# Kernel tuning notes

Hardware: AMD Instinct MI355X
Metric: run time of the kernel (lower is better)

The kernel has to match this reference:

```python
import jax, jax.numpy as jnp
import numpy as np
import math

NHEAD = 8
OUT = 64
EF = 64
IN = 256
NTYPES = 5
NH = 50000
NT = 100000
E = 800000
NEG_SLOPE = 0.2

def _uniform(key, shape, fan):
    # matches reset(): uniform(-stdv, stdv), stdv = sqrt(6/(fan_in+fan_out)) over last two dims
    stdv = math.sqrt(6.0 / (shape[-2] + shape[-1]))
    return jax.random.uniform(key, shape, jnp.float32, -stdv, stdv)

def setup_inputs() -> dict:
    key = jax.random.key(0)
    ks = jax.random.split(key, 12)
    head_feature = jax.random.normal(ks[0], (NH, IN), jnp.float32)
    tail_feature = jax.random.normal(ks[1], (NT, IN), jnp.float32)
    head_ind = jax.random.randint(ks[2], (E,), 0, NH)
    tail_ind = jax.random.randint(ks[3], (E,), 0, NT)
    tmp_edge = jax.random.randint(ks[4], (E,), 0, NTYPES)
    edge_emb = _uniform(ks[5], (NTYPES, EF), None)
    W = _uniform(ks[6], (IN, OUT * NHEAD), None)
    W_e = _uniform(ks[7], (EF, EF * NHEAD), None)
    a_l = _uniform(ks[8], (1, NHEAD, OUT), None)
    a_r = _uniform(ks[9], (1, NHEAD, OUT), None)
    a_e = _uniform(ks[10], (1, NHEAD, EF), None)
    return {"head_feature": head_feature, "tail_feature": tail_feature,
            "head_ind": head_ind, "tail_ind": tail_ind, "tmp_edge": tmp_edge,
            "edge_emb": edge_emb, "W": W, "W_e": W_e,
            "a_l": a_l, "a_r": a_r, "a_e": a_e}

def reference(head_feature, tail_feature, head_ind, tail_ind, tmp_edge,
              edge_emb, W, W_e, a_l, a_r, a_e):
    n_head_nodes = head_feature.shape[0]
    # projections (dropout is identity in eval)
    h_head = (head_feature @ W).reshape(-1, NHEAD, OUT)   # [NH, H, D]
    h_tail = (tail_feature @ W).reshape(-1, NHEAD, OUT)   # [NT, H, D]
    e = (edge_emb @ W_e).reshape(-1, NHEAD, EF)           # [T, H, EF]
    # per-edge attention logits, all heads at once: [E, H]
    h_l = jnp.sum(a_l * h_head, axis=-1)[head_ind]
    h_r = jnp.sum(a_r * h_tail, axis=-1)[tail_ind]
    h_e = jnp.sum(a_e * e, axis=-1)[tmp_edge]
    att = jax.nn.leaky_relu(h_l + h_r + h_e, NEG_SLOPE)
    # sparse (per-destination-row) softmax, vectorized over heads
    seg_max = jax.ops.segment_max(att, head_ind, num_segments=n_head_nodes)
    att = jnp.exp(att - seg_max[head_ind])
    denom = jax.ops.segment_sum(att, head_ind, num_segments=n_head_nodes)
    att = att / denom[head_ind]                           # [E, H]
    # weighted aggregation per head (small fixed loop over heads)
    outs = [jax.ops.segment_sum(att[:, n:n + 1] * h_tail[tail_ind, n, :],
                                head_ind, num_segments=n_head_nodes)
            for n in range(NHEAD)]
    out = jnp.stack(outs, axis=1).reshape(n_head_nodes, -1)  # [NH, H*D]
    return out, att
```

## Files before the change

kernel.cpp:

```cpp
#include <hip/hip_runtime.h>

#define NH 50000
#define NT 100000
#define NE 800000
#define MPAD 100096

typedef __attribute__((ext_vector_type(8))) short bf16x8;
typedef __attribute__((ext_vector_type(4))) float f32x4;
typedef __attribute__((ext_vector_type(8))) unsigned short u16x8;

__device__ __forceinline__ unsigned short f2bf(float f){
  unsigned int u = __float_as_uint(f);
  u += 0x7FFFu + ((u >> 16) & 1u);
  return (unsigned short)(u >> 16);
}

__device__ __forceinline__ void fma8(float* acc, float w, uint4 pk){
  acc[0] += w*__uint_as_float(pk.x<<16); acc[1] += w*__uint_as_float(pk.x&0xFFFF0000u);
  acc[2] += w*__uint_as_float(pk.y<<16); acc[3] += w*__uint_as_float(pk.y&0xFFFF0000u);
  acc[4] += w*__uint_as_float(pk.z<<16); acc[5] += w*__uint_as_float(pk.z&0xFFFF0000u);
  acc[6] += w*__uint_as_float(pk.w<<16); acc[7] += w*__uint_as_float(pk.w&0xFFFF0000u);
}

__device__ __forceinline__ void gl2lds16(const unsigned short* g, unsigned short* l){
  __builtin_amdgcn_global_load_lds(
      (const __attribute__((address_space(1))) void*)g,
      (__attribute__((address_space(3))) void*)l, 16, 0, 0);
}

__global__ void k_prep(const float* __restrict__ W, const float* __restrict__ W_e,
                       const float* __restrict__ edge_emb,
                       const float* __restrict__ a_l, const float* __restrict__ a_r,
                       const float* __restrict__ a_e,
                       unsigned short* __restrict__ wlr_t,
                       float* __restrict__ h_e){
  __shared__ float s_al[512], s_ar[512], s_ae[512], s_wef[512];
  int t = threadIdx.x;
  for (int i=t;i<512;i+=256){ s_al[i]=a_l[i]; s_ar[i]=a_r[i]; s_ae[i]=a_e[i]; }
  __syncthreads();
  { int k = t;
    for (int h=0;h<8;h++){
      float accl=0.f, accr=0.f;
      for (int d=0; d<64; d++){
        float w = W[k*512 + h*64 + d];
        accl += w*s_al[h*64+d];
        accr += w*s_ar[h*64+d];
      }
      wlr_t[h*256 + k]     = f2bf(accl);
      wlr_t[(8+h)*256 + k] = f2bf(accr);
    }
  }
  if (t<64){
    for (int h=0;h<8;h++){
      float acc=0.f;
      for (int f=0; f<64; f++) acc += W_e[t*512 + h*64 + f]*s_ae[h*64+f];
      s_wef[t*8+h]=acc;
    }
  }
  __syncthreads();
  if (t<40){
    int ty=t>>3, h=t&7;
    float acc=0.f;
    for (int k2=0;k2<64;k2++) acc += edge_emb[ty*64+k2]*s_wef[k2*8+h];
    h_e[t]=acc;
  }
}

__global__ void k_wt(const float* __restrict__ W, unsigned short* __restrict__ Wt){
  int n = blockIdx.x, k = threadIdx.x;
  Wt[n*256+k] = f2bf(W[k*512+n]);
}

__global__ __launch_bounds__(256) void k_cvt(const float* __restrict__ A,
                                             unsigned short* __restrict__ Ab){
  size_t g = (size_t)blockIdx.x*256 + threadIdx.x;
  const float* src = A + g*8;
  float4 v0 = *(const float4*)(src);
  float4 v1 = *(const float4*)(src + 4);
  u16x8 s;
  s[0]=f2bf(v0.x); s[1]=f2bf(v0.y); s[2]=f2bf(v0.z); s[3]=f2bf(v0.w);
  s[4]=f2bf(v1.x); s[5]=f2bf(v1.y); s[6]=f2bf(v1.z); s[7]=f2bf(v1.w);
  *(u16x8*)(Ab + g*8) = s;
}

__global__ __launch_bounds__(256) void k_hl(const float* __restrict__ head_f,
      const unsigned short* __restrict__ wlr_t, float* __restrict__ h_l){
  __shared__ unsigned short As[256*64];
  __shared__ unsigned short Bs[16*256];
  int t = threadIdx.x;
  int wave = t>>6, lane = t&63;
  int lr = lane&15, lq = lane>>4;
  long r0 = (long)blockIdx.x*256;

#pragma unroll
  for (int i=0;i<2;i++){
    int q = i*256 + t;
    int c = q>>5, un = q&31;
    float4 v = *(const float4*)(wlr_t + c*256 + un*8);
    int u = un ^ (c&7);
    *(float4*)((char*)Bs + c*512 + u*16) = v;
  }

  f32x4 acc[4];
#pragma unroll
  for (int mf=0;mf<4;mf++) acc[mf]=(f32x4){0.f,0.f,0.f,0.f};

  for (int kt=0; kt<4; kt++){
    __syncthreads();
#pragma unroll
    for (int i=0;i<16;i++){
      int q = i*256+t;
      int row = q>>4, cg = q&15;
      long gr = r0 + row;
      float4 v = make_float4(0.f,0.f,0.f,0.f);
      if (gr < NH) v = *(const float4*)(head_f + gr*256 + kt*64 + cg*4);
      int u = (cg>>1) ^ (row&7);
      ushort4 sv;
      sv.x=f2bf(v.x); sv.y=f2bf(v.y); sv.z=f2bf(v.z); sv.w=f2bf(v.w);
      *(ushort4*)((char*)As + row*128 + u*16 + (cg&1)*8) = sv;
    }
    __syncthreads();
#pragma unroll
    for (int ks=0;ks<2;ks++){
      int un = kt*8 + ks*4 + lq;
      int cu = un ^ (lr&7);
      bf16x8 bfr = *(const bf16x8*)((const char*)Bs + lr*512 + cu*16);
#pragma unroll
      for (int mf=0;mf<4;mf++){
        int r = wave*64 + mf*16 + lr;
        int u = (ks*4+lq) ^ (r&7);
        bf16x8 afr = *(const bf16x8*)((const char*)As + r*128 + u*16);
        acc[mf] = __builtin_amdgcn_mfma_f32_16x16x32_bf16(afr, bfr, acc[mf], 0,0,0);
      }
    }
  }
#pragma unroll
  for (int mf=0;mf<4;mf++)
#pragma unroll
    for (int j=0;j<4;j++){
      long grow = r0 + wave*64 + mf*16 + lq*4 + j;
      if (grow < NH && lr < 8) h_l[grow*8+lr] = acc[mf][j];
    }
}

__global__ __launch_bounds__(256) void k_gemm2(const unsigned short* __restrict__ A_bf,
      const unsigned short* __restrict__ Wt, const float* __restrict__ a_r_g,
      unsigned short* __restrict__ Cout, float* __restrict__ h_r){
  __shared__ unsigned short As[2][128*64];
  __shared__ unsigned short Bs[2][128*64];
  int t = threadIdx.x;
  int wave = t>>6, lane = t&63;
  int lr = lane & 15, lq = lane >> 4;

  int bid = blockIdx.x;
  int wg  = (bid & 7)*391 + (bid >> 3);
  int m0 = (wg >> 2)*128;
  int n0 = (wg & 3)*128;

  auto STAGE = [&](int buf, int kt){
#pragma unroll
    for (int i=0;i<4;i++){
      int v = wave*256 + i*64 + lane;
      int row = v>>3, un = (v&7) ^ (row&7);
      gl2lds16(A_bf + (size_t)(m0+row)*256 + kt*64 + un*8,
               &As[buf][(wave*256 + i*64)*8]);
    }
#pragma unroll
    for (int i=0;i<4;i++){
      int v = wave*256 + i*64 + lane;
      int n = v>>3, un = (v&7) ^ (n&7);
      gl2lds16(Wt + (size_t)(n0+n)*256 + kt*64 + un*8,
               &Bs[buf][(wave*256 + i*64)*8]);
    }
  };

  int wm = (wave>>1)*64, wn = (wave&1)*64;

  f32x4 acc[4][4];
#pragma unroll
  for (int mf=0;mf<4;mf++)
#pragma unroll
    for (int nf=0;nf<4;nf++) acc[mf][nf] = (f32x4){0.f,0.f,0.f,0.f};

  STAGE(0, 0);
  __syncthreads();
  int cur = 0;
  for (int kt=0; kt<4; kt++){
    if (kt < 3) STAGE(cur^1, kt+1);

    bf16x8 af[2][4], bfr[2][4];
#pragma unroll
    for (int ks=0;ks<2;ks++)
#pragma unroll
      for (int mf=0;mf<4;mf++){
        int r = wm + mf*16 + lr;
        int u = (ks*4 + lq) ^ (r&7);
        af[ks][mf] = *(const bf16x8*)((const char*)As[cur] + r*128 + u*16);
      }
#pragma unroll
    for (int ks=0;ks<2;ks++)
#pragma unroll
      for (int nf=0;nf<4;nf++){
        int c = wn + nf*16 + lr;
        int u = (ks*4 + lq) ^ (c&7);
        bfr[ks][nf] = *(const bf16x8*)((const char*)Bs[cur] + c*128 + u*16);
      }
#pragma unroll
    for (int ks=0;ks<2;ks++)
#pragma unroll
      for (int mf=0;mf<4;mf++)
#pragma unroll
        for (int nf=0;nf<4;nf++)
          acc[mf][nf] = __builtin_amdgcn_mfma_f32_16x16x32_bf16(af[ks][mf], bfr[ks][nf], acc[mf][nf], 0,0,0);
    __syncthreads();
    cur ^= 1;
  }
#pragma unroll
  for (int mf=0;mf<4;mf++)
#pragma unroll
    for (int nf=0;nf<4;nf++){
      int gr = m0 + wm + mf*16 + lq*4;
      int gc = n0 + wn + nf*16 + lr;
#pragma unroll
      for (int j=0;j<4;j++)
        Cout[(size_t)(gr+j)*512 + gc] = f2bf(acc[mf][nf][j]);
    }
  {
    int h = (n0 + wn) >> 6;
    float w[4];
#pragma unroll
    for (int nf=0;nf<4;nf++) w[nf] = a_r_g[h*64 + nf*16 + lr];
#pragma unroll
    for (int mf=0;mf<4;mf++)
#pragma unroll
      for (int j=0;j<4;j++){
        float s = acc[mf][0][j]*w[0] + acc[mf][1][j]*w[1]
                + acc[mf][2][j]*w[2] + acc[mf][3][j]*w[3];
        s += __shfl_xor(s, 1); s += __shfl_xor(s, 2);
        s += __shfl_xor(s, 4); s += __shfl_xor(s, 8);
        int gr = m0 + wm + mf*16 + lq*4 + j;
        if (lr == 0 && gr < NT) h_r[(size_t)gr*8 + h] = s;
      }
  }
}

__global__ void k_hist(const int* __restrict__ head_ind, int* __restrict__ cnt){
  int e = blockIdx.x*256 + threadIdx.x;
  atomicAdd(&cnt[head_ind[e]], 1);
}

__global__ void k_scan1(const int* __restrict__ cnt, int* __restrict__ bsum){
  __shared__ int s[256];
  int b=blockIdx.x, t=threadIdx.x, g=b*256+t;
  s[t] = (g<NH)? cnt[g] : 0;
  __syncthreads();
  for (int off=128; off>0; off>>=1){ if (t<off) s[t]+=s[t+off]; __syncthreads(); }
  if (t==0) bsum[b]=s[0];
}
__global__ void k_scan2(int* __restrict__ bsum, int nb){
  __shared__ int s[256];
  int t=threadIdx.x;
  int v = (t<nb)? bsum[t] : 0;
  s[t]=v; __syncthreads();
  for (int off=1; off<256; off<<=1){
    int u = (t>=off)? s[t-off] : 0; __syncthreads();
    s[t]+=u; __syncthreads();
  }
  if (t<nb) bsum[t] = s[t]-v;
}
__global__ void k_scan3(const int* __restrict__ cnt, const int* __restrict__ bsum,
                        int* __restrict__ offs, int* __restrict__ cur){
  __shared__ int s[256];
  int b=blockIdx.x, t=threadIdx.x, g=b*256+t;
  int v=(g<NH)? cnt[g] : 0;
  s[t]=v; __syncthreads();
  for (int off=1; off<256; off<<=1){
    int u=(t>=off)? s[t-off] : 0; __syncthreads();
    s[t]+=u; __syncthreads();
  }
  int excl = s[t]-v + bsum[b];
  if (g<NH){
    offs[g]=excl; cur[g]=excl;
    if (g==NH-1) offs[NH]=excl+v;
  }
}

__global__ void k_logit2(const int* __restrict__ head_ind, const int* __restrict__ tail_ind,
                         const int* __restrict__ tmp_edge,
                         const float* __restrict__ h_l, const float* __restrict__ h_r,
                         const float* __restrict__ h_e,
                         int* __restrict__ cur,
                         float* __restrict__ att_csr,
                         int* __restrict__ edge_of, int* __restrict__ tail_s){
  int g = blockIdx.x*256 + threadIdx.x;
  int e = g>>3, h = g&7, l = threadIdx.x&63;
  int hd = head_ind[e], tl = tail_ind[e], ty = tmp_edge[e];
  float v = h_l[hd*8+h] + h_r[(size_t)tl*8+h] + h_e[ty*8+h];
  v = v > 0.f ? v : 0.2f*v;
  int p = 0;
  if (h==0) p = atomicAdd(&cur[hd], 1);
  p = __shfl(p, l & ~7);
  att_csr[p*8+h] = v;
  if (h==0){ edge_of[p]=e; tail_s[p]=tl; }
}

__global__ __launch_bounds__(256) void k_agg3(const int* __restrict__ offs,
      const int* __restrict__ edge_of, const int* __restrict__ tail_s,
      const float* __restrict__ att_csr,
      const unsigned short* __restrict__ h_tail,
      float* __restrict__ att, float* __restrict__ out){
  int t = threadIdx.x;
  int l = t & 63;
  int i = blockIdx.x*4 + (t>>6);
  int h = l & 7, hq = l >> 3;
  int s0 = offs[i];
  int deg = offs[i+1] - s0;

  float m = -1e30f;
  for (int q = hq; q < deg; q += 8) m = fmaxf(m, att_csr[(s0+q)*8 + h]);
  m = fmaxf(m, __shfl_xor(m, 8));
  m = fmaxf(m, __shfl_xor(m, 16));
  m = fmaxf(m, __shfl_xor(m, 32));
  float sum = 0.f;
  for (int q = hq; q < deg; q += 8) sum += __expf(att_csr[(s0+q)*8 + h] - m);
  sum += __shfl_xor(sum, 8); sum += __shfl_xor(sum, 16); sum += __shfl_xor(sum, 32);
  float r = (deg > 0) ? 1.f/sum : 0.f;

  float mh = __shfl(m, hq), rh = __shfl(r, hq);
  bool wlane = (l & 7) == 0;
  float acc[8];
#pragma unroll
  for (int c=0;c<8;c++) acc[c]=0.f;
  int j = 0;
  for (; j+4 <= deg; j += 4){
    int p0=s0+j, p1=p0+1, p2=p0+2, p3=p0+3;
    int t0=tail_s[p0], t1=tail_s[p1], t2=tail_s[p2], t3=tail_s[p3];
    float a0=att_csr[p0*8+hq], a1=att_csr[p1*8+hq];
    float a2=att_csr[p2*8+hq], a3=att_csr[p3*8+hq];
    uint4 r0 = *(const uint4*)(h_tail + (size_t)t0*512 + l*8);
    uint4 r1 = *(const uint4*)(h_tail + (size_t)t1*512 + l*8);
    uint4 r2 = *(const uint4*)(h_tail + (size_t)t2*512 + l*8);
    uint4 r3 = *(const uint4*)(h_tail + (size_t)t3*512 + l*8);
    float w0=__expf(a0-mh)*rh, w1=__expf(a1-mh)*rh;
    float w2=__expf(a2-mh)*rh, w3=__expf(a3-mh)*rh;
    if (wlane){
      __builtin_nontemporal_store(w0, &att[(size_t)edge_of[p0]*8 + hq]);
      __builtin_nontemporal_store(w1, &att[(size_t)edge_of[p1]*8 + hq]);
      __builtin_nontemporal_store(w2, &att[(size_t)edge_of[p2]*8 + hq]);
      __builtin_nontemporal_store(w3, &att[(size_t)edge_of[p3]*8 + hq]);
    }
    fma8(acc, w0, r0);
    fma8(acc, w1, r1);
    fma8(acc, w2, r2);
    fma8(acc, w3, r3);
  }
  for (; j < deg; j++){
    int p0 = s0+j;
    int t0 = tail_s[p0];
    float a0 = att_csr[p0*8 + hq];
    uint4 r0 = *(const uint4*)(h_tail + (size_t)t0*512 + l*8);
    float w0 = __expf(a0 - mh) * rh;
    if (wlane) __builtin_nontemporal_store(w0, &att[(size_t)edge_of[p0]*8 + hq]);
    fma8(acc, w0, r0);
  }
  float* o = out + (size_t)i*512 + l*8;
  f32x4 v0 = {acc[0],acc[1],acc[2],acc[3]};
  f32x4 v1 = {acc[4],acc[5],acc[6],acc[7]};
  __builtin_nontemporal_store(v0, (f32x4*)o);
  __builtin_nontemporal_store(v1, (f32x4*)(o+4));
}

extern "C" void kernel_launch(void* const* d_in, const int* in_sizes, int n_in,
                              void* d_out, int out_size, void* d_ws, size_t ws_size,
                              hipStream_t stream) {
  const float* head_f   = (const float*)d_in[0];
  const float* tail_f   = (const float*)d_in[1];
  const int*   head_ind = (const int*)d_in[2];
  const int*   tail_ind = (const int*)d_in[3];
  const int*   tmp_edge = (const int*)d_in[4];
  const float* edge_emb = (const float*)d_in[5];
  const float* W        = (const float*)d_in[6];
  const float* W_e      = (const float*)d_in[7];
  const float* a_l      = (const float*)d_in[8];
  const float* a_r      = (const float*)d_in[9];
  const float* a_e      = (const float*)d_in[10];

  float* out = (float*)d_out;
  float* att = out + (size_t)NH*512;
  unsigned short* A_bf = (unsigned short*)d_out;

  char* ws = (char*)d_ws;
  auto alloc = [&](size_t bytes)->char*{ char* p = ws; ws += (bytes+511)&~(size_t)511; return p; };
  unsigned short* Wt    = (unsigned short*)alloc((size_t)512*256*2);
  unsigned short* wlr_t = (unsigned short*)alloc((size_t)16*256*2);
  float* h_e            = (float*)alloc(512);
  float* h_l            = (float*)alloc((size_t)NH*8*4);
  float* h_r            = (float*)alloc((size_t)NT*8*4);
  unsigned short* h_tail= (unsigned short*)alloc((size_t)MPAD*512*2);
  int* cnt              = (int*)alloc((size_t)NH*4);
  int* offs             = (int*)alloc((size_t)(NH+1)*4);
  int* cur              = (int*)alloc((size_t)NH*4);
  int* bsum             = (int*)alloc(1024);
  int* edge_of          = (int*)alloc((size_t)NE*4);
  int* tail_s           = (int*)alloc((size_t)NE*4);
  float* att_csr        = (float*)alloc((size_t)NE*8*4);

  hipMemsetAsync(cnt, 0, (size_t)NH*4, stream);
  k_prep<<<1,256,0,stream>>>(W, W_e, edge_emb, a_l, a_r, a_e, wlr_t, h_e);
  k_wt<<<512,256,0,stream>>>(W, Wt);
  k_cvt<<<12500,256,0,stream>>>(tail_f, A_bf);
  k_hl<<<(NH+255)/256,256,0,stream>>>(head_f, wlr_t, h_l);
  k_gemm2<<<3128,256,0,stream>>>(A_bf, Wt, a_r, h_tail, h_r);
  k_hist<<<NE/256,256,0,stream>>>(head_ind, cnt);
  k_scan1<<<196,256,0,stream>>>(cnt, bsum);
  k_scan2<<<1,256,0,stream>>>(bsum, 196);
  k_scan3<<<196,256,0,stream>>>(cnt, bsum, offs, cur);
  k_logit2<<<NE*8/256,256,0,stream>>>(head_ind, tail_ind, tmp_edge, h_l, h_r, h_e,
                                      cur, att_csr, edge_of, tail_s);
  k_agg3<<<NH/4,256,0,stream>>>(offs, edge_of, tail_s, att_csr, h_tail, att, out);
}
```

Before: 436.8 us.

## Load GEMM B operand to registers, stage C via LDS, deepen gather unroll

The tail GEMM now reads the W operand straight from global memory into registers, prefetching the next k-tile, and no longer stages it through LDS. This halves shared memory use and drops the B-side LDS reads. The GEMM output is written through a swizzled LDS tile so it can be stored as coalesced 16-byte rows instead of scattered 2-byte stores. The aggregation loop is unrolled to 8 edges, with all gathers issued before any use, to raise memory-level parallelism. The cost is higher register pressure in both kernels, and B fragments are reloaded per wave from L2 rather than shared.

```diff
diff --git a/kernel.cpp b/kernel.cpp
--- a/kernel.cpp
+++ b/kernel.cpp
@@ -143,11 +143,10 @@
     }
 }
 
-__global__ __launch_bounds__(256) void k_gemm2(const unsigned short* __restrict__ A_bf,
+__global__ __launch_bounds__(256) void k_gemm3(const unsigned short* __restrict__ A_bf,
       const unsigned short* __restrict__ Wt, const float* __restrict__ a_r_g,
       unsigned short* __restrict__ Cout, float* __restrict__ h_r){
   __shared__ unsigned short As[2][128*64];
-  __shared__ unsigned short Bs[2][128*64];
   int t = threadIdx.x;
   int wave = t>>6, lane = t&63;
   int lr = lane & 15, lq = lane >> 4;
@@ -156,24 +155,6 @@
   int wg  = (bid & 7)*391 + (bid >> 3);
   int m0 = (wg >> 2)*128;
   int n0 = (wg & 3)*128;
-
-  auto STAGE = [&](int buf, int kt){
-#pragma unroll
-    for (int i=0;i<4;i++){
-      int v = wave*256 + i*64 + lane;
-      int row = v>>3, un = (v&7) ^ (row&7);
-      gl2lds16(A_bf + (size_t)(m0+row)*256 + kt*64 + un*8,
-               &As[buf][(wave*256 + i*64)*8]);
-    }
-#pragma unroll
-    for (int i=0;i<4;i++){
-      int v = wave*256 + i*64 + lane;
-      int n = v>>3, un = (v&7) ^ (n&7);
-      gl2lds16(Wt + (size_t)(n0+n)*256 + kt*64 + un*8,
-               &Bs[buf][(wave*256 + i*64)*8]);
-    }
-  };
-
   int wm = (wave>>1)*64, wn = (wave&1)*64;
 
   f32x4 acc[4][4];
@@ -182,49 +163,57 @@
 #pragma unroll
     for (int nf=0;nf<4;nf++) acc[mf][nf] = (f32x4){0.f,0.f,0.f,0.f};
 
-  STAGE(0, 0);
+  bf16x8 bcur[8], bnxt[8];
+
+#define STAGEA(buf, kt) do { \
+    _Pragma("unroll") \
+    for (int i=0;i<4;i++){ \
+      int v = wave*256 + i*64 + lane; \
+      int row = v>>3, un = (v&7) ^ (row&7); \
+      gl2lds16(A_bf + (size_t)(m0+row)*256 + (kt)*64 + un*8, \
+               &As[buf][(wave*256 + i*64)*8]); \
+    } } while(0)
+
+#define LOADB(kt, dst) do { \
+    _Pragma("unroll") \
+    for (int ks=0;ks<2;ks++) \
+      _Pragma("unroll") \
+      for (int nf=0;nf<4;nf++){ \
+        int c = wn + nf*16 + lr; \
+        (dst)[ks*4+nf] = *(const bf16x8*)(Wt + (size_t)(n0+c)*256 + ((kt)*8+ks*4+lq)*8); \
+      } } while(0)
+
+  STAGEA(0, 0);
+  LOADB(0, bcur);
   __syncthreads();
   int cur = 0;
   for (int kt=0; kt<4; kt++){
-    if (kt < 3) STAGE(cur^1, kt+1);
-
-    bf16x8 af[2][4], bfr[2][4];
-#pragma unroll
-    for (int ks=0;ks<2;ks++)
+    if (kt < 3){ STAGEA(cur^1, kt+1); LOADB(kt+1, bnxt); }
+#pragma unroll
+    for (int ks=0;ks<2;ks++){
+      bf16x8 af[4];
 #pragma unroll
       for (int mf=0;mf<4;mf++){
         int r = wm + mf*16 + lr;
         int u = (ks*4 + lq) ^ (r&7);
-        af[ks][mf] = *(const bf16x8*)((const char*)As[cur] + r*128 + u*16);
+        af[mf] = *(const bf16x8*)((const char*)As[cur] + r*128 + u*16);
       }
 #pragma unroll
-    for (int ks=0;ks<2;ks++)
-#pragma unroll
-      for (int nf=0;nf<4;nf++){
-        int c = wn + nf*16 + lr;
-        int u = (ks*4 + lq) ^ (c&7);
-        bfr[ks][nf] = *(const bf16x8*)((const char*)Bs[cur] + c*128 + u*16);
-      }
-#pragma unroll
-    for (int ks=0;ks<2;ks++)
-#pragma unroll
       for (int mf=0;mf<4;mf++)
 #pragma unroll
         for (int nf=0;nf<4;nf++)
-          acc[mf][nf] = __builtin_amdgcn_mfma_f32_16x16x32_bf16(af[ks][mf], bfr[ks][nf], acc[mf][nf], 0,0,0);
+          acc[mf][nf] = __builtin_amdgcn_mfma_f32_16x16x32_bf16(af[mf], bcur[ks*4+nf], acc[mf][nf], 0,0,0);
+    }
     __syncthreads();
-    cur ^= 1;
-  }
-#pragma unroll
-  for (int mf=0;mf<4;mf++)
-#pragma unroll
-    for (int nf=0;nf<4;nf++){
-      int gr = m0 + wm + mf*16 + lq*4;
-      int gc = n0 + wn + nf*16 + lr;
-#pragma unroll
-      for (int j=0;j<4;j++)
-        Cout[(size_t)(gr+j)*512 + gc] = f2bf(acc[mf][nf][j]);
-    }
+    if (kt < 3){
+      cur ^= 1;
+#pragma unroll
+      for (int i=0;i<8;i++) bcur[i] = bnxt[i];
+    }
+  }
+#undef STAGEA
+#undef LOADB
+
   {
     int h = (n0 + wn) >> 6;
     float w[4];
@@ -241,6 +230,26 @@
         int gr = m0 + wm + mf*16 + lq*4 + j;
         if (lr == 0 && gr < NT) h_r[(size_t)gr*8 + h] = s;
       }
+  }
+
+  unsigned short* Cs = &As[0][0];
+#pragma unroll
+  for (int mf=0;mf<4;mf++)
+#pragma unroll
+    for (int nf=0;nf<4;nf++)
+#pragma unroll
+      for (int j=0;j<4;j++){
+        int row = wm + mf*16 + lq*4 + j;
+        int cb  = (wn + nf*16 + lr)*2;
+        *(unsigned short*)((char*)Cs + row*256 + (cb ^ ((row&12)<<3))) = f2bf(acc[mf][nf][j]);
+      }
+  __syncthreads();
+#pragma unroll
+  for (int i=0;i<8;i++){
+    int v = i*256 + t;
+    int row = v>>4, u = v&15;
+    uint4 val = *(const uint4*)((const char*)Cs + row*256 + ((u*16) ^ ((row&12)<<3)));
+    *(uint4*)(Cout + (size_t)(m0+row)*512 + n0 + u*8) = val;
   }
 }
 
@@ -331,30 +340,36 @@
   float acc[8];
 #pragma unroll
   for (int c=0;c<8;c++) acc[c]=0.f;
+
   int j = 0;
-  for (; j+4 <= deg; j += 4){
-    int p0=s0+j, p1=p0+1, p2=p0+2, p3=p0+3;
-    int t0=tail_s[p0], t1=tail_s[p1], t2=tail_s[p2], t3=tail_s[p3];
+  for (; j+8 <= deg; j += 8){
+    int   tt[8]; float aa[8]; uint4 rr[8];
+#pragma unroll
+    for (int q2=0;q2<8;q2++){ int p=s0+j+q2; tt[q2]=tail_s[p]; aa[q2]=att_csr[p*8+hq]; }
+#pragma unroll
+    for (int q2=0;q2<8;q2++) rr[q2] = *(const uint4*)(h_tail + (size_t)tt[q2]*512 + l*8);
+#pragma unroll
+    for (int q2=0;q2<8;q2++){
+      float w = __expf(aa[q2]-mh)*rh;
+      if (wlane) __builtin_nontemporal_store(w, &att[(size_t)edge_of[s0+j+q2]*8 + hq]);
+      fma8(acc, w, rr[q2]);
+    }
+  }
+  for (; j+2 <= deg; j += 2){
+    int p0=s0+j, p1=p0+1;
+    int t0=tail_s[p0], t1=tail_s[p1];
     float a0=att_csr[p0*8+hq], a1=att_csr[p1*8+hq];
-    float a2=att_csr[p2*8+hq], a3=att_csr[p3*8+hq];
     uint4 r0 = *(const uint4*)(h_tail + (size_t)t0*512 + l*8);
     uint4 r1 = *(const uint4*)(h_tail + (size_t)t1*512 + l*8);
-    uint4 r2 = *(const uint4*)(h_tail + (size_t)t2*512 + l*8);
-    uint4 r3 = *(const uint4*)(h_tail + (size_t)t3*512 + l*8);
     float w0=__expf(a0-mh)*rh, w1=__expf(a1-mh)*rh;
-    float w2=__expf(a2-mh)*rh, w3=__expf(a3-mh)*rh;
     if (wlane){
       __builtin_nontemporal_store(w0, &att[(size_t)edge_of[p0]*8 + hq]);
       __builtin_nontemporal_store(w1, &att[(size_t)edge_of[p1]*8 + hq]);
-      __builtin_nontemporal_store(w2, &att[(size_t)edge_of[p2]*8 + hq]);
-      __builtin_nontemporal_store(w3, &att[(size_t)edge_of[p3]*8 + hq]);
     }
     fma8(acc, w0, r0);
     fma8(acc, w1, r1);
-    fma8(acc, w2, r2);
-    fma8(acc, w3, r3);
-  }
-  for (; j < deg; j++){
+  }
+  if (j < deg){
     int p0 = s0+j;
     int t0 = tail_s[p0];
     float a0 = att_csr[p0*8 + hq];
@@ -410,7 +425,7 @@
   k_wt<<<512,256,0,stream>>>(W, Wt);
   k_cvt<<<12500,256,0,stream>>>(tail_f, A_bf);
   k_hl<<<(NH+255)/256,256,0,stream>>>(head_f, wlr_t, h_l);
-  k_gemm2<<<3128,256,0,stream>>>(A_bf, Wt, a_r, h_tail, h_r);
+  k_gemm3<<<3128,256,0,stream>>>(A_bf, Wt, a_r, h_tail, h_r);
   k_hist<<<NE/256,256,0,stream>>>(head_ind, cnt);
   k_scan1<<<196,256,0,stream>>>(cnt, bsum);
   k_scan2<<<1,256,0,stream>>>(bsum, 196);
```

New measurement: 438.5 us. No clear change (+0.4%).

## Load GEMM operands directly from global into registers and stage output through LDS

Applied to the files above, without the earlier changes.

The tail-projection GEMM drops its double-buffered LDS staging of A and B tiles. MFMA fragments are now loaded straight from global memory into registers over a fully unrolled K loop, with launch bounds raised for occupancy. The bf16 output is written into a swizzled LDS tile and then stored with coalesced 16-byte writes, replacing the scattered 2-byte stores. This removes LDS traffic and barriers in the main loop, but relies on L1/L2 to serve the redundant global fragment reads across waves.

```diff
diff --git a/kernel.cpp b/kernel.cpp
--- a/kernel.cpp
+++ b/kernel.cpp
@@ -8,6 +8,7 @@
 typedef __attribute__((ext_vector_type(8))) short bf16x8;
 typedef __attribute__((ext_vector_type(4))) float f32x4;
 typedef __attribute__((ext_vector_type(8))) unsigned short u16x8;
+typedef __attribute__((ext_vector_type(4))) unsigned int u32x4;
 
 __device__ __forceinline__ unsigned short f2bf(float f){
   unsigned int u = __float_as_uint(f);
@@ -20,12 +21,6 @@
   acc[2] += w*__uint_as_float(pk.y<<16); acc[3] += w*__uint_as_float(pk.y&0xFFFF0000u);
   acc[4] += w*__uint_as_float(pk.z<<16); acc[5] += w*__uint_as_float(pk.z&0xFFFF0000u);
   acc[6] += w*__uint_as_float(pk.w<<16); acc[7] += w*__uint_as_float(pk.w&0xFFFF0000u);
-}
-
-__device__ __forceinline__ void gl2lds16(const unsigned short* g, unsigned short* l){
-  __builtin_amdgcn_global_load_lds(
-      (const __attribute__((address_space(1))) void*)g,
-      (__attribute__((address_space(3))) void*)l, 16, 0, 0);
 }
 
 __global__ void k_prep(const float* __restrict__ W, const float* __restrict__ W_e,
@@ -143,11 +138,10 @@
     }
 }
 
-__global__ __launch_bounds__(256) void k_gemm2(const unsigned short* __restrict__ A_bf,
+__global__ __launch_bounds__(256,4) void k_gemm5(const unsigned short* __restrict__ A_bf,
       const unsigned short* __restrict__ Wt, const float* __restrict__ a_r_g,
       unsigned short* __restrict__ Cout, float* __restrict__ h_r){
-  __shared__ unsigned short As[2][128*64];
-  __shared__ unsigned short Bs[2][128*64];
+  __shared__ unsigned short Cs[128*128];
   int t = threadIdx.x;
   int wave = t>>6, lane = t&63;
   int lr = lane & 15, lq = lane >> 4;
@@ -156,75 +150,33 @@
   int wg  = (bid & 7)*391 + (bid >> 3);
   int m0 = (wg >> 2)*128;
   int n0 = (wg & 3)*128;
-
-  auto STAGE = [&](int buf, int kt){
-#pragma unroll
-    for (int i=0;i<4;i++){
-      int v = wave*256 + i*64 + lane;
-      int row = v>>3, un = (v&7) ^ (row&7);
-      gl2lds16(A_bf + (size_t)(m0+row)*256 + kt*64 + un*8,
-               &As[buf][(wave*256 + i*64)*8]);
-    }
-#pragma unroll
-    for (int i=0;i<4;i++){
-      int v = wave*256 + i*64 + lane;
-      int n = v>>3, un = (v&7) ^ (n&7);
-      gl2lds16(Wt + (size_t)(n0+n)*256 + kt*64 + un*8,
-               &Bs[buf][(wave*256 + i*64)*8]);
-    }
-  };
-
   int wm = (wave>>1)*64, wn = (wave&1)*64;
 
+  const unsigned short* Abase = A_bf + (size_t)(m0 + wm)*256;
+  const unsigned short* Bbase = Wt  + (size_t)(n0 + wn)*256;
+
   f32x4 acc[4][4];
 #pragma unroll
   for (int mf=0;mf<4;mf++)
 #pragma unroll
     for (int nf=0;nf<4;nf++) acc[mf][nf] = (f32x4){0.f,0.f,0.f,0.f};
 
-  STAGE(0, 0);
-  __syncthreads();
-  int cur = 0;
-  for (int kt=0; kt<4; kt++){
-    if (kt < 3) STAGE(cur^1, kt+1);
-
-    bf16x8 af[2][4], bfr[2][4];
-#pragma unroll
-    for (int ks=0;ks<2;ks++)
-#pragma unroll
-      for (int mf=0;mf<4;mf++){
-        int r = wm + mf*16 + lr;
-        int u = (ks*4 + lq) ^ (r&7);
-        af[ks][mf] = *(const bf16x8*)((const char*)As[cur] + r*128 + u*16);
-      }
-#pragma unroll
-    for (int ks=0;ks<2;ks++)
-#pragma unroll
-      for (int nf=0;nf<4;nf++){
-        int c = wn + nf*16 + lr;
-        int u = (ks*4 + lq) ^ (c&7);
-        bfr[ks][nf] = *(const bf16x8*)((const char*)Bs[cur] + c*128 + u*16);
-      }
-#pragma unroll
-    for (int ks=0;ks<2;ks++)
-#pragma unroll
-      for (int mf=0;mf<4;mf++)
-#pragma unroll
-        for (int nf=0;nf<4;nf++)
-          acc[mf][nf] = __builtin_amdgcn_mfma_f32_16x16x32_bf16(af[ks][mf], bfr[ks][nf], acc[mf][nf], 0,0,0);
-    __syncthreads();
-    cur ^= 1;
-  }
-#pragma unroll
-  for (int mf=0;mf<4;mf++)
-#pragma unroll
-    for (int nf=0;nf<4;nf++){
-      int gr = m0 + wm + mf*16 + lq*4;
-      int gc = n0 + wn + nf*16 + lr;
-#pragma unroll
-      for (int j=0;j<4;j++)
-        Cout[(size_t)(gr+j)*512 + gc] = f2bf(acc[mf][nf][j]);
-    }
+#pragma unroll
+  for (int ks=0; ks<8; ks++){
+    bf16x8 af[4], bfr[4];
+#pragma unroll
+    for (int mf=0;mf<4;mf++)
+      af[mf] = *(const bf16x8*)(Abase + (size_t)(mf*16+lr)*256 + ks*32 + lq*8);
+#pragma unroll
+    for (int nf=0;nf<4;nf++)
+      bfr[nf] = *(const bf16x8*)(Bbase + (size_t)(nf*16+lr)*256 + ks*32 + lq*8);
+#pragma unroll
+    for (int mf=0;mf<4;mf++)
+#pragma unroll
+      for (int nf=0;nf<4;nf++)
+        acc[mf][nf] = __builtin_amdgcn_mfma_f32_16x16x32_bf16(af[mf], bfr[nf], acc[mf][nf], 0,0,0);
+  }
+
   {
     int h = (n0 + wn) >> 6;
     float w[4];
@@ -241,6 +193,25 @@
         int gr = m0 + wm + mf*16 + lq*4 + j;
         if (lr == 0 && gr < NT) h_r[(size_t)gr*8 + h] = s;
       }
+  }
+
+#pragma unroll
+  for (int mf=0;mf<4;mf++)
+#pragma unroll
+    for (int nf=0;nf<4;nf++)
+#pragma unroll
+      for (int j=0;j<4;j++){
+        int row = wm + mf*16 + lq*4 + j;
+        int cb  = (wn + nf*16 + lr)*2;
+        *(unsigned short*)((char*)Cs + row*256 + (cb ^ ((row&12)<<3))) = f2bf(acc[mf][nf][j]);
+      }
+  __syncthreads();
+#pragma unroll
+  for (int i=0;i<8;i++){
+    int v = i*256 + t;
+    int row = v>>4, u = v&15;
+    u32x4 val = *(const u32x4*)((const char*)Cs + row*256 + ((u*16) ^ ((row&12)<<3)));
+    *(u32x4*)(Cout + (size_t)(m0+row)*512 + n0 + u*8) = val;
   }
 }
 
@@ -410,7 +381,7 @@
   k_wt<<<512,256,0,stream>>>(W, Wt);
   k_cvt<<<12500,256,0,stream>>>(tail_f, A_bf);
   k_hl<<<(NH+255)/256,256,0,stream>>>(head_f, wlr_t, h_l);
-  k_gemm2<<<3128,256,0,stream>>>(A_bf, Wt, a_r, h_tail, h_r);
+  k_gemm5<<<3128,256,0,stream>>>(A_bf, Wt, a_r, h_tail, h_r);
   k_hist<<<NE/256,256,0,stream>>>(head_ind, cnt);
   k_scan1<<<196,256,0,stream>>>(cnt, bsum);
   k_scan2<<<1,256,0,stream>>>(bsum, 196);
```

Measured after the change: 476.9 us. 9.2% more time.
